# Kernel tuning notes

Hardware: AMD Instinct MI355X
Metric: run time of the kernel (lower is better)

Reference implementation:

```python
import jax, jax.numpy as jnp
import numpy as np

BN_EPS = 1e-5


def _gin_layer(x, src, dst, n_nodes, W1, b1, W2, b2, gamma, beta):
    # GINConv with eps=0: z_i = x_i + sum_{(j->i) in E} x_j, then 2-layer MLP
    agg = jax.ops.segment_sum(x[src], dst, num_segments=n_nodes)  # [N, d]
    z = x + agg
    z = jax.nn.relu(z @ W1 + b1) @ W2 + b2
    # BatchNorm1d (training mode: biased batch statistics over node dim)
    mean = jnp.mean(z, axis=0)
    var = jnp.var(z, axis=0)
    z = (z - mean) * jax.lax.rsqrt(var + BN_EPS) * gamma + beta
    return jax.nn.relu(z)  # dropout p=0 -> identity


def setup_inputs() -> dict:
    key = jax.random.key(0)
    ks = jax.random.split(key, 8)
    N, E, D, L = 50000, 800000, 128, 2
    h = jax.random.normal(ks[0], (N, D), dtype=jnp.float32)
    edge_index = jax.random.randint(ks[1], (2, E), 0, N, dtype=jnp.int64)
    scale = 1.0 / np.sqrt(D)
    W1 = jax.random.normal(ks[2], (L, D, D), dtype=jnp.float32) * scale
    b1 = jax.random.normal(ks[3], (L, D), dtype=jnp.float32) * 0.01
    W2 = jax.random.normal(ks[4], (L, D, D), dtype=jnp.float32) * scale
    b2 = jax.random.normal(ks[5], (L, D), dtype=jnp.float32) * 0.01
    gamma = jnp.ones((L, D), dtype=jnp.float32)
    beta = jnp.zeros((L, D), dtype=jnp.float32)
    return {"h": h, "edge_index": edge_index, "W1": W1, "b1": b1,
            "W2": W2, "b2": b2, "gamma": gamma, "beta": beta}


def reference(h, edge_index, W1, b1, W2, b2, gamma, beta):
    src, dst = edge_index[0], edge_index[1]
    n_nodes = h.shape[0]
    n_layers = W1.shape[0]
    outs = []
    x = h
    for i in range(n_layers):
        x = _gin_layer(x, src, dst, n_nodes, W1[i], b1[i], W2[i], b2[i], gamma[i], beta[i])
        outs.append(x)
    return jnp.stack(outs)  # [L, N, D] == hs[1:]
```

## Files before the change

kernel.cpp:

```cpp
#include <hip/hip_runtime.h>

#define D 128
#define BN_EPS 1e-5f

typedef __attribute__((ext_vector_type(8))) short short8;
typedef __attribute__((ext_vector_type(4))) float f32x4;

__device__ inline unsigned short f2bf(float f) {
    union { float f; unsigned int u; } v; v.f = f;
    unsigned int u = v.u;
    unsigned int r = (u + 0x7FFFu + ((u >> 16) & 1u)) >> 16;
    return (unsigned short)r;
}

__device__ inline float bfbits2f(unsigned int bits) {
    union { unsigned int u; float f; } v; v.u = bits;
    return v.f;
}

__device__ inline float4 bf2f4(uint2 v) {
    float4 r;
    r.x = bfbits2f(v.x << 16);
    r.y = bfbits2f(v.x & 0xFFFF0000u);
    r.z = bfbits2f(v.y << 16);
    r.w = bfbits2f(v.y & 0xFFFF0000u);
    return r;
}

__global__ void hist_rank(const int* __restrict__ dst, int* __restrict__ cnt,
                          int* __restrict__ rank, int E) {
    int e = blockIdx.x * blockDim.x + threadIdx.x;
    if (e >= E) return;
    rank[e] = atomicAdd(&cnt[dst[e]], 1);
}

__global__ void reduce_cnt(const int* __restrict__ cnt, int* __restrict__ bsum, int n) {
    __shared__ int s[256];
    int tid = threadIdx.x;
    int i = blockIdx.x * 256 + tid;
    s[tid] = (i < n) ? cnt[i] : 0;
    __syncthreads();
    for (int ofs = 128; ofs > 0; ofs >>= 1) {
        if (tid < ofs) s[tid] += s[tid + ofs];
        __syncthreads();
    }
    if (tid == 0) bsum[blockIdx.x] = s[0];
}

__global__ void scan_bsums(const int* __restrict__ bsum, int* __restrict__ blockOff,
                           int* __restrict__ offN, int nb) {
    __shared__ int s[256];
    int tid = threadIdx.x;
    int v = (tid < nb) ? bsum[tid] : 0;
    s[tid] = v;
    __syncthreads();
    for (int ofs = 1; ofs < 256; ofs <<= 1) {
        int t = (tid >= ofs) ? s[tid - ofs] : 0;
        __syncthreads();
        s[tid] += t;
        __syncthreads();
    }
    if (tid < nb) blockOff[tid] = s[tid] - v;
    if (tid == nb - 1) *offN = s[tid];
}

__global__ void scan_partial(const int* __restrict__ cnt, int* __restrict__ off,
                             const int* __restrict__ blockOff, int n) {
    __shared__ int s[256];
    int tid = threadIdx.x;
    int i = blockIdx.x * 256 + tid;
    int v = (i < n) ? cnt[i] : 0;
    s[tid] = v;
    __syncthreads();
    for (int ofs = 1; ofs < 256; ofs <<= 1) {
        int t = (tid >= ofs) ? s[tid - ofs] : 0;
        __syncthreads();
        s[tid] += t;
        __syncthreads();
    }
    if (i < n) off[i] = blockOff[blockIdx.x] + s[tid] - v;
}

template<typename IdxT>
__global__ void fill2(const int* __restrict__ src, const int* __restrict__ dst,
                      const int* __restrict__ rank, const int* __restrict__ off,
                      IdxT* __restrict__ eidx, int E) {
    int e = blockIdx.x * blockDim.x + threadIdx.x;
    if (e >= E) return;
    eidx[off[dst[e]] + rank[e]] = (IdxT)src[e];
}

__global__ void wprep(const float* __restrict__ W1, const float* __restrict__ W2,
                      unsigned short* __restrict__ Wt, int L) {
    int idx = blockIdx.x * 256 + threadIdx.x;
    int m = idx >> 14;
    int rem = idx & 16383;
    int c = rem >> 7, k = rem & 127;
    const float* W = (m < L) ? (W1 + (size_t)m * D * D) : (W2 + (size_t)(m - L) * D * D);
    Wt[(size_t)m * D * D + c * D + k] = f2bf(W[k * D + c]);
}

__global__ void x2bf(const float* __restrict__ x, unsigned short* __restrict__ xb, int n8) {
    int i = blockIdx.x * 256 + threadIdx.x;
    if (i >= n8) return;
    float4 a = reinterpret_cast<const float4*>(x)[2 * i];
    float4 b = reinterpret_cast<const float4*>(x)[2 * i + 1];
    uint4 o;
    o.x = (unsigned)f2bf(a.x) | ((unsigned)f2bf(a.y) << 16);
    o.y = (unsigned)f2bf(a.z) | ((unsigned)f2bf(a.w) << 16);
    o.z = (unsigned)f2bf(b.x) | ((unsigned)f2bf(b.y) << 16);
    o.w = (unsigned)f2bf(b.z) | ((unsigned)f2bf(b.w) << 16);
    reinterpret_cast<uint4*>(xb)[i] = o;
}

template<typename IdxT>
__global__ __launch_bounds__(256) void gather_bf(
        const unsigned short* __restrict__ xb, const int* __restrict__ off,
        const IdxT* __restrict__ eidx, unsigned short* __restrict__ zb, int N) {
    int t = blockIdx.x * blockDim.x + threadIdx.x;
    int node = t >> 5;
    if (node >= N) return;
    int lane = t & 31;
    int beg = off[node], end = off[node + 1];
    float4 acc = bf2f4(*reinterpret_cast<const uint2*>(xb + (size_t)node * D + lane * 4));
    int e = beg;
    for (; e + 2 <= end; e += 2) {
        int s0 = (int)eidx[e], s1 = (int)eidx[e + 1];
        uint2 v0 = *reinterpret_cast<const uint2*>(xb + (size_t)s0 * D + lane * 4);
        uint2 v1 = *reinterpret_cast<const uint2*>(xb + (size_t)s1 * D + lane * 4);
        float4 f0 = bf2f4(v0), f1 = bf2f4(v1);
        acc.x += f0.x + f1.x; acc.y += f0.y + f1.y;
        acc.z += f0.z + f1.z; acc.w += f0.w + f1.w;
    }
    if (e < end) {
        int s0 = (int)eidx[e];
        float4 f0 = bf2f4(*reinterpret_cast<const uint2*>(xb + (size_t)s0 * D + lane * 4));
        acc.x += f0.x; acc.y += f0.y; acc.z += f0.z; acc.w += f0.w;
    }
    uint2 o;
    o.x = (unsigned)f2bf(acc.x) | ((unsigned)f2bf(acc.y) << 16);
    o.y = (unsigned)f2bf(acc.z) | ((unsigned)f2bf(acc.w) << 16);
    *reinterpret_cast<uint2*>(zb + (size_t)node * D + lane * 4) = o;
}

__global__ __launch_bounds__(256) void gemm1_mfma(
        const unsigned short* __restrict__ A, const unsigned short* __restrict__ Wt,
        const float* __restrict__ bias, unsigned short* __restrict__ Out, int N) {
    const int tid = threadIdx.x;
    const int lane = tid & 63, wv = tid >> 6;
    const int r0 = blockIdx.x * 128 + wv * 32;
    const int koff = (lane >> 4) << 3;
    const int col = lane & 15;

    int ar0 = r0 + col;       if (ar0 >= N) ar0 = N - 1;
    int ar1 = r0 + 16 + col;  if (ar1 >= N) ar1 = N - 1;
    const unsigned short* ap0 = A + (size_t)ar0 * D + koff;
    const unsigned short* ap1 = A + (size_t)ar1 * D + koff;
    const unsigned short* wp  = Wt + (size_t)col * D + koff;

    f32x4 acc[2][8];
    #pragma unroll
    for (int ct = 0; ct < 8; ct++) {
        float b = bias[ct * 16 + col];
        acc[0][ct] = (f32x4){b, b, b, b};
        acc[1][ct] = (f32x4){b, b, b, b};
    }
    #pragma unroll
    for (int ks = 0; ks < 4; ks++) {
        short8 a0 = *reinterpret_cast<const short8*>(ap0 + ks * 32);
        short8 a1 = *reinterpret_cast<const short8*>(ap1 + ks * 32);
        #pragma unroll
        for (int ct = 0; ct < 8; ct++) {
            short8 bfr = *reinterpret_cast<const short8*>(wp + (size_t)ct * 16 * D + ks * 32);
            acc[0][ct] = __builtin_amdgcn_mfma_f32_16x16x32_bf16(a0, bfr, acc[0][ct], 0, 0, 0);
            acc[1][ct] = __builtin_amdgcn_mfma_f32_16x16x32_bf16(a1, bfr, acc[1][ct], 0, 0, 0);
        }
    }
    #pragma unroll
    for (int t = 0; t < 2; t++) {
        #pragma unroll
        for (int ct = 0; ct < 8; ct++) {
            #pragma unroll
            for (int r = 0; r < 4; r++) {
                int row = r0 + t * 16 + ((lane >> 4) << 2) + r;
                if (row < N)
                    Out[(size_t)row * D + ct * 16 + col] = f2bf(fmaxf(acc[t][ct][r], 0.f));
            }
        }
    }
}

__global__ __launch_bounds__(256) void gemm2_mfma(
        const unsigned short* __restrict__ A, const unsigned short* __restrict__ Wt,
        const float* __restrict__ bias, float* __restrict__ Out,
        float* __restrict__ gstats, int N) {
    __shared__ float sStat[2 * D];
    const int tid = threadIdx.x;
    if (tid < 2 * D) sStat[tid] = 0.f;
    __syncthreads();

    const int lane = tid & 63, wv = tid >> 6;
    const int r0 = blockIdx.x * 128 + wv * 32;
    const int koff = (lane >> 4) << 3;
    const int col = lane & 15;

    int ar0 = r0 + col;       if (ar0 >= N) ar0 = N - 1;
    int ar1 = r0 + 16 + col;  if (ar1 >= N) ar1 = N - 1;
    const unsigned short* ap0 = A + (size_t)ar0 * D + koff;
    const unsigned short* ap1 = A + (size_t)ar1 * D + koff;
    const unsigned short* wp  = Wt + (size_t)col * D + koff;

    f32x4 acc[2][8];
    #pragma unroll
    for (int ct = 0; ct < 8; ct++) {
        float b = bias[ct * 16 + col];
        acc[0][ct] = (f32x4){b, b, b, b};
        acc[1][ct] = (f32x4){b, b, b, b};
    }
    #pragma unroll
    for (int ks = 0; ks < 4; ks++) {
        short8 a0 = *reinterpret_cast<const short8*>(ap0 + ks * 32);
        short8 a1 = *reinterpret_cast<const short8*>(ap1 + ks * 32);
        #pragma unroll
        for (int ct = 0; ct < 8; ct++) {
            short8 bfr = *reinterpret_cast<const short8*>(wp + (size_t)ct * 16 * D + ks * 32);
            acc[0][ct] = __builtin_amdgcn_mfma_f32_16x16x32_bf16(a0, bfr, acc[0][ct], 0, 0, 0);
            acc[1][ct] = __builtin_amdgcn_mfma_f32_16x16x32_bf16(a1, bfr, acc[1][ct], 0, 0, 0);
        }
    }
    #pragma unroll
    for (int ct = 0; ct < 8; ct++) {
        float s = 0.f, q = 0.f;
        #pragma unroll
        for (int t = 0; t < 2; t++) {
            #pragma unroll
            for (int r = 0; r < 4; r++) {
                int row = r0 + t * 16 + ((lane >> 4) << 2) + r;
                float v = acc[t][ct][r];
                if (row < N) {
                    Out[(size_t)row * D + ct * 16 + col] = v;
                    s += v; q += v * v;
                }
            }
        }
        s += __shfl_xor(s, 16); q += __shfl_xor(q, 16);
        s += __shfl_xor(s, 32); q += __shfl_xor(q, 32);
        if (lane < 16) {
            atomicAdd(&sStat[ct * 16 + lane], s);
            atomicAdd(&sStat[D + ct * 16 + lane], q);
        }
    }
    __syncthreads();
    if (tid < 2 * D) atomicAdd(&gstats[tid], sStat[tid]);
}

__global__ void bn_relu_bf(float* __restrict__ y, unsigned short* __restrict__ xb,
                           const float* __restrict__ stats,
                           const float* __restrict__ gamma, const float* __restrict__ beta,
                           int N, int emit_bf) {
    int i = blockIdx.x * blockDim.x + threadIdx.x;
    int n4 = N * D / 4;
    if (i >= n4) return;
    int c0 = (i << 2) & (D - 1);
    float4 v = reinterpret_cast<float4*>(y)[i];
    float o[4] = {v.x, v.y, v.z, v.w};
    float invN = 1.0f / (float)N;
    #pragma unroll
    for (int j = 0; j < 4; j++) {
        int c = c0 + j;
        float mean = stats[c] * invN;
        float var  = stats[D + c] * invN - mean * mean;
        float sc = rsqrtf(var + BN_EPS) * gamma[c];
        float t = (o[j] - mean) * sc + beta[c];
        o[j] = fmaxf(t, 0.f);
    }
    float4 r; r.x = o[0]; r.y = o[1]; r.z = o[2]; r.w = o[3];
    reinterpret_cast<float4*>(y)[i] = r;
    if (emit_bf) {
        uint2 ob;
        ob.x = (unsigned)f2bf(o[0]) | ((unsigned)f2bf(o[1]) << 16);
        ob.y = (unsigned)f2bf(o[2]) | ((unsigned)f2bf(o[3]) << 16);
        reinterpret_cast<uint2*>(xb)[i] = ob;
    }
}

extern "C" void kernel_launch(void* const* d_in, const int* in_sizes, int n_in,
                              void* d_out, int out_size, void* d_ws, size_t ws_size,
                              hipStream_t stream) {
    const float* h     = (const float*)d_in[0];
    const int*   ei    = (const int*)d_in[1];
    const float* W1    = (const float*)d_in[2];
    const float* b1    = (const float*)d_in[3];
    const float* W2    = (const float*)d_in[4];
    const float* b2    = (const float*)d_in[5];
    const float* gamma = (const float*)d_in[6];
    const float* beta  = (const float*)d_in[7];
    float* out = (float*)d_out;

    const int N = in_sizes[0] / D;
    const int E = in_sizes[1] / 2;
    const int L = in_sizes[2] / (D * D);
    const int nb = (N + 255) / 256;

    unsigned short* zb  = (unsigned short*)d_ws;
    unsigned short* xb  = zb + (size_t)N * D;
    unsigned short* Wt  = xb + (size_t)N * D;
    float* stats = (float*)(Wt + (size_t)2 * L * D * D);
    int* cnt      = (int*)(stats + (size_t)L * 2 * D);
    int* off      = cnt + N;
    int* bsum     = off + N + 1;
    int* blockOff = bsum + nb;
    int* rank     = blockOff + nb;
    void* eidx    = (void*)(rank + E);

    const int* src = ei;
    const int* dst = ei + E;

    const int n4 = N * D / 4;
    const int n8 = N * D / 8;
    const int ewBlocks = (E + 255) / 256;
    const int gatherBlocks = (N * 32 + 255) / 256;
    const int gemmBlocks = (N + 127) / 128;
    const int bnBlocks = (n4 + 255) / 256;
    const int wprepBlocks = (2 * L * D * D) / 256;
    const bool small = (N <= 65535);

    hipMemsetAsync(cnt, 0, N * sizeof(int), stream);
    hipMemsetAsync(stats, 0, (size_t)L * 2 * D * sizeof(float), stream);
    wprep<<<wprepBlocks, 256, 0, stream>>>(W1, W2, Wt, L);
    x2bf<<<(n8 + 255) / 256, 256, 0, stream>>>(h, xb, n8);

    hist_rank<<<ewBlocks, 256, 0, stream>>>(dst, cnt, rank, E);
    reduce_cnt<<<nb, 256, 0, stream>>>(cnt, bsum, N);
    scan_bsums<<<1, 256, 0, stream>>>(bsum, blockOff, off + N, nb);
    scan_partial<<<nb, 256, 0, stream>>>(cnt, off, blockOff, N);
    if (small)
        fill2<unsigned short><<<ewBlocks, 256, 0, stream>>>(src, dst, rank, off,
                                                            (unsigned short*)eidx, E);
    else
        fill2<int><<<ewBlocks, 256, 0, stream>>>(src, dst, rank, off, (int*)eidx, E);

    for (int l = 0; l < L; l++) {
        float* y = out + (size_t)l * N * D;

        if (small)
            gather_bf<unsigned short><<<gatherBlocks, 256, 0, stream>>>(
                xb, off, (const unsigned short*)eidx, zb, N);
        else
            gather_bf<int><<<gatherBlocks, 256, 0, stream>>>(
                xb, off, (const int*)eidx, zb, N);
        gemm1_mfma<<<gemmBlocks, 256, 0, stream>>>(zb, Wt + (size_t)l * D * D,
                                                   b1 + (size_t)l * D, zb, N);
        gemm2_mfma<<<gemmBlocks, 256, 0, stream>>>(zb, Wt + (size_t)(L + l) * D * D,
                                                   b2 + (size_t)l * D, y, stats + (size_t)l * 2 * D, N);
        bn_relu_bf<<<bnBlocks, 256, 0, stream>>>(y, xb, stats + (size_t)l * 2 * D,
                                                 gamma + (size_t)l * D, beta + (size_t)l * D,
                                                 N, (l + 1 < L) ? 1 : 0);
    }
}
```

Before: 240.5 us.

## Fuse neighbor gather and both MLP GEMMs into one kernel via LDS tile

Replaces the separate gather, gemm1 and gemm2 kernels with one fused kernel per layer. Each block gathers 128 node rows into a swizzled 32KB LDS tile, runs the first GEMM with ReLU back into LDS, then runs the second GEMM and accumulates BN statistics. This removes the global round trips of the aggregated and hidden bf16 activations and two launches per layer. In exchange, occupancy drops because of the large LDS use and high register pressure, and the irregular gather phase gets less latency hiding, since each wave now walks 16 rows serially.

```diff
diff --git a/kernel.cpp b/kernel.cpp
--- a/kernel.cpp
+++ b/kernel.cpp
@@ -114,66 +114,78 @@
 }
 
 template<typename IdxT>
-__global__ __launch_bounds__(256) void gather_bf(
+__global__ __launch_bounds__(256) void fused_layer(
         const unsigned short* __restrict__ xb, const int* __restrict__ off,
-        const IdxT* __restrict__ eidx, unsigned short* __restrict__ zb, int N) {
-    int t = blockIdx.x * blockDim.x + threadIdx.x;
-    int node = t >> 5;
-    if (node >= N) return;
-    int lane = t & 31;
-    int beg = off[node], end = off[node + 1];
-    float4 acc = bf2f4(*reinterpret_cast<const uint2*>(xb + (size_t)node * D + lane * 4));
-    int e = beg;
-    for (; e + 2 <= end; e += 2) {
-        int s0 = (int)eidx[e], s1 = (int)eidx[e + 1];
-        uint2 v0 = *reinterpret_cast<const uint2*>(xb + (size_t)s0 * D + lane * 4);
-        uint2 v1 = *reinterpret_cast<const uint2*>(xb + (size_t)s1 * D + lane * 4);
-        float4 f0 = bf2f4(v0), f1 = bf2f4(v1);
-        acc.x += f0.x + f1.x; acc.y += f0.y + f1.y;
-        acc.z += f0.z + f1.z; acc.w += f0.w + f1.w;
-    }
-    if (e < end) {
-        int s0 = (int)eidx[e];
-        float4 f0 = bf2f4(*reinterpret_cast<const uint2*>(xb + (size_t)s0 * D + lane * 4));
-        acc.x += f0.x; acc.y += f0.y; acc.z += f0.z; acc.w += f0.w;
-    }
-    uint2 o;
-    o.x = (unsigned)f2bf(acc.x) | ((unsigned)f2bf(acc.y) << 16);
-    o.y = (unsigned)f2bf(acc.z) | ((unsigned)f2bf(acc.w) << 16);
-    *reinterpret_cast<uint2*>(zb + (size_t)node * D + lane * 4) = o;
-}
-
-__global__ __launch_bounds__(256) void gemm1_mfma(
-        const unsigned short* __restrict__ A, const unsigned short* __restrict__ Wt,
-        const float* __restrict__ bias, unsigned short* __restrict__ Out, int N) {
+        const IdxT* __restrict__ eidx,
+        const unsigned short* __restrict__ Wt1, const float* __restrict__ b1,
+        const unsigned short* __restrict__ Wt2, const float* __restrict__ b2,
+        float* __restrict__ Out, float* __restrict__ gstats, int N) {
+    __shared__ __align__(16) char sZ[128 * 256];
+    __shared__ float sStat[2 * D];
     const int tid = threadIdx.x;
     const int lane = tid & 63, wv = tid >> 6;
-    const int r0 = blockIdx.x * 128 + wv * 32;
-    const int koff = (lane >> 4) << 3;
+    const int row0 = blockIdx.x * 128;
+
+    sStat[tid] = 0.f;
+
+    {
+        const int lane32 = lane & 31;
+        const int sub = lane >> 5;
+        for (int it = 0; it < 16; it++) {
+            int lrow = wv * 32 + it * 2 + sub;
+            int node = row0 + lrow;
+            float4 acc = make_float4(0.f, 0.f, 0.f, 0.f);
+            if (node < N) {
+                acc = bf2f4(*reinterpret_cast<const uint2*>(xb + (size_t)node * D + lane32 * 4));
+                int beg = off[node], end = off[node + 1];
+                int e = beg;
+                for (; e + 2 <= end; e += 2) {
+                    int s0 = (int)eidx[e], s1 = (int)eidx[e + 1];
+                    float4 f0 = bf2f4(*reinterpret_cast<const uint2*>(xb + (size_t)s0 * D + lane32 * 4));
+                    float4 f1 = bf2f4(*reinterpret_cast<const uint2*>(xb + (size_t)s1 * D + lane32 * 4));
+                    acc.x += f0.x + f1.x; acc.y += f0.y + f1.y;
+                    acc.z += f0.z + f1.z; acc.w += f0.w + f1.w;
+                }
+                if (e < end) {
+                    int s0 = (int)eidx[e];
+                    float4 f0 = bf2f4(*reinterpret_cast<const uint2*>(xb + (size_t)s0 * D + lane32 * 4));
+                    acc.x += f0.x; acc.y += f0.y; acc.z += f0.z; acc.w += f0.w;
+                }
+            }
+            uint2 o;
+            o.x = (unsigned)f2bf(acc.x) | ((unsigned)f2bf(acc.y) << 16);
+            o.y = (unsigned)f2bf(acc.z) | ((unsigned)f2bf(acc.w) << 16);
+            *reinterpret_cast<uint2*>(sZ + lrow * 256 + ((lane32 * 8) ^ ((lrow & 7) << 4))) = o;
+        }
+    }
+    __syncthreads();
+
     const int col = lane & 15;
-
-    int ar0 = r0 + col;       if (ar0 >= N) ar0 = N - 1;
-    int ar1 = r0 + 16 + col;  if (ar1 >= N) ar1 = N - 1;
-    const unsigned short* ap0 = A + (size_t)ar0 * D + koff;
-    const unsigned short* ap1 = A + (size_t)ar1 * D + koff;
-    const unsigned short* wp  = Wt + (size_t)col * D + koff;
-
-    f32x4 acc[2][8];
+    const int kq = lane >> 4;
+    const int lrow0 = wv * 32 + col;
+    const int lrow1 = wv * 32 + 16 + col;
+
+    f32x4 acc1[2][8];
     #pragma unroll
     for (int ct = 0; ct < 8; ct++) {
-        float b = bias[ct * 16 + col];
-        acc[0][ct] = (f32x4){b, b, b, b};
-        acc[1][ct] = (f32x4){b, b, b, b};
-    }
-    #pragma unroll
-    for (int ks = 0; ks < 4; ks++) {
-        short8 a0 = *reinterpret_cast<const short8*>(ap0 + ks * 32);
-        short8 a1 = *reinterpret_cast<const short8*>(ap1 + ks * 32);
+        float b = b1[ct * 16 + col];
+        acc1[0][ct] = (f32x4){b, b, b, b};
+        acc1[1][ct] = (f32x4){b, b, b, b};
+    }
+    {
+        const unsigned short* wp = Wt1 + (size_t)col * D + kq * 8;
         #pragma unroll
-        for (int ct = 0; ct < 8; ct++) {
-            short8 bfr = *reinterpret_cast<const short8*>(wp + (size_t)ct * 16 * D + ks * 32);
-            acc[0][ct] = __builtin_amdgcn_mfma_f32_16x16x32_bf16(a0, bfr, acc[0][ct], 0, 0, 0);
-            acc[1][ct] = __builtin_amdgcn_mfma_f32_16x16x32_bf16(a1, bfr, acc[1][ct], 0, 0, 0);
+        for (int ks = 0; ks < 4; ks++) {
+            short8 a0 = *reinterpret_cast<const short8*>(
+                sZ + lrow0 * 256 + ((kq * 16 + ks * 64) ^ ((lrow0 & 7) << 4)));
+            short8 a1 = *reinterpret_cast<const short8*>(
+                sZ + lrow1 * 256 + ((kq * 16 + ks * 64) ^ ((lrow1 & 7) << 4)));
+            #pragma unroll
+            for (int ct = 0; ct < 8; ct++) {
+                short8 bfr = *reinterpret_cast<const short8*>(wp + (size_t)ct * 16 * D + ks * 32);
+                acc1[0][ct] = __builtin_amdgcn_mfma_f32_16x16x32_bf16(a0, bfr, acc1[0][ct], 0, 0, 0);
+                acc1[1][ct] = __builtin_amdgcn_mfma_f32_16x16x32_bf16(a1, bfr, acc1[1][ct], 0, 0, 0);
+            }
         }
     }
     #pragma unroll
@@ -182,50 +194,36 @@
         for (int ct = 0; ct < 8; ct++) {
             #pragma unroll
             for (int r = 0; r < 4; r++) {
-                int row = r0 + t * 16 + ((lane >> 4) << 2) + r;
-                if (row < N)
-                    Out[(size_t)row * D + ct * 16 + col] = f2bf(fmaxf(acc[t][ct][r], 0.f));
-            }
-        }
-    }
-}
-
-__global__ __launch_bounds__(256) void gemm2_mfma(
-        const unsigned short* __restrict__ A, const unsigned short* __restrict__ Wt,
-        const float* __restrict__ bias, float* __restrict__ Out,
-        float* __restrict__ gstats, int N) {
-    __shared__ float sStat[2 * D];
-    const int tid = threadIdx.x;
-    if (tid < 2 * D) sStat[tid] = 0.f;
-    __syncthreads();
-
-    const int lane = tid & 63, wv = tid >> 6;
-    const int r0 = blockIdx.x * 128 + wv * 32;
-    const int koff = (lane >> 4) << 3;
-    const int col = lane & 15;
-
-    int ar0 = r0 + col;       if (ar0 >= N) ar0 = N - 1;
-    int ar1 = r0 + 16 + col;  if (ar1 >= N) ar1 = N - 1;
-    const unsigned short* ap0 = A + (size_t)ar0 * D + koff;
-    const unsigned short* ap1 = A + (size_t)ar1 * D + koff;
-    const unsigned short* wp  = Wt + (size_t)col * D + koff;
-
-    f32x4 acc[2][8];
+                int lrow = wv * 32 + t * 16 + kq * 4 + r;
+                int c = ct * 16 + col;
+                unsigned short hv = f2bf(fmaxf(acc1[t][ct][r], 0.f));
+                *reinterpret_cast<unsigned short*>(
+                    sZ + lrow * 256 + ((c * 2) ^ ((lrow & 7) << 4))) = hv;
+            }
+        }
+    }
+
+    f32x4 acc2[2][8];
     #pragma unroll
     for (int ct = 0; ct < 8; ct++) {
-        float b = bias[ct * 16 + col];
-        acc[0][ct] = (f32x4){b, b, b, b};
-        acc[1][ct] = (f32x4){b, b, b, b};
-    }
-    #pragma unroll
-    for (int ks = 0; ks < 4; ks++) {
-        short8 a0 = *reinterpret_cast<const short8*>(ap0 + ks * 32);
-        short8 a1 = *reinterpret_cast<const short8*>(ap1 + ks * 32);
+        float b = b2[ct * 16 + col];
+        acc2[0][ct] = (f32x4){b, b, b, b};
+        acc2[1][ct] = (f32x4){b, b, b, b};
+    }
+    {
+        const unsigned short* wp = Wt2 + (size_t)col * D + kq * 8;
         #pragma unroll
-        for (int ct = 0; ct < 8; ct++) {
-            short8 bfr = *reinterpret_cast<const short8*>(wp + (size_t)ct * 16 * D + ks * 32);
-            acc[0][ct] = __builtin_amdgcn_mfma_f32_16x16x32_bf16(a0, bfr, acc[0][ct], 0, 0, 0);
-            acc[1][ct] = __builtin_amdgcn_mfma_f32_16x16x32_bf16(a1, bfr, acc[1][ct], 0, 0, 0);
+        for (int ks = 0; ks < 4; ks++) {
+            short8 a0 = *reinterpret_cast<const short8*>(
+                sZ + lrow0 * 256 + ((kq * 16 + ks * 64) ^ ((lrow0 & 7) << 4)));
+            short8 a1 = *reinterpret_cast<const short8*>(
+                sZ + lrow1 * 256 + ((kq * 16 + ks * 64) ^ ((lrow1 & 7) << 4)));
+            #pragma unroll
+            for (int ct = 0; ct < 8; ct++) {
+                short8 bfr = *reinterpret_cast<const short8*>(wp + (size_t)ct * 16 * D + ks * 32);
+                acc2[0][ct] = __builtin_amdgcn_mfma_f32_16x16x32_bf16(a0, bfr, acc2[0][ct], 0, 0, 0);
+                acc2[1][ct] = __builtin_amdgcn_mfma_f32_16x16x32_bf16(a1, bfr, acc2[1][ct], 0, 0, 0);
+            }
         }
     }
     #pragma unroll
@@ -235,8 +233,8 @@
         for (int t = 0; t < 2; t++) {
             #pragma unroll
             for (int r = 0; r < 4; r++) {
-                int row = r0 + t * 16 + ((lane >> 4) << 2) + r;
-                float v = acc[t][ct][r];
+                int row = row0 + wv * 32 + t * 16 + kq * 4 + r;
+                float v = acc2[t][ct][r];
                 if (row < N) {
                     Out[(size_t)row * D + ct * 16 + col] = v;
                     s += v; q += v * v;
@@ -251,7 +249,7 @@
         }
     }
     __syncthreads();
-    if (tid < 2 * D) atomicAdd(&gstats[tid], sStat[tid]);
+    atomicAdd(&gstats[tid], sStat[tid]);
 }
 
 __global__ void bn_relu_bf(float* __restrict__ y, unsigned short* __restrict__ xb,
@@ -302,8 +300,7 @@
     const int L = in_sizes[2] / (D * D);
     const int nb = (N + 255) / 256;
 
-    unsigned short* zb  = (unsigned short*)d_ws;
-    unsigned short* xb  = zb + (size_t)N * D;
+    unsigned short* xb  = (unsigned short*)d_ws;
     unsigned short* Wt  = xb + (size_t)N * D;
     float* stats = (float*)(Wt + (size_t)2 * L * D * D);
     int* cnt      = (int*)(stats + (size_t)L * 2 * D);
@@ -319,8 +316,7 @@
     const int n4 = N * D / 4;
     const int n8 = N * D / 8;
     const int ewBlocks = (E + 255) / 256;
-    const int gatherBlocks = (N * 32 + 255) / 256;
-    const int gemmBlocks = (N + 127) / 128;
+    const int fusedBlocks = (N + 127) / 128;
     const int bnBlocks = (n4 + 255) / 256;
     const int wprepBlocks = (2 * L * D * D) / 256;
     const bool small = (N <= 65535);
@@ -342,17 +338,18 @@
 
     for (int l = 0; l < L; l++) {
         float* y = out + (size_t)l * N * D;
+        const unsigned short* Wt1 = Wt + (size_t)l * D * D;
+        const unsigned short* Wt2 = Wt + (size_t)(L + l) * D * D;
 
         if (small)
-            gather_bf<unsigned short><<<gatherBlocks, 256, 0, stream>>>(
-                xb, off, (const unsigned short*)eidx, zb, N);
+            fused_layer<unsigned short><<<fusedBlocks, 256, 0, stream>>>(
+                xb, off, (const unsigned short*)eidx, Wt1, b1 + (size_t)l * D,
+                Wt2, b2 + (size_t)l * D, y, stats + (size_t)l * 2 * D, N);
         else
-            gather_bf<int><<<gatherBlocks, 256, 0, stream>>>(
-                xb, off, (const int*)eidx, zb, N);
-        gemm1_mfma<<<gemmBlocks, 256, 0, stream>>>(zb, Wt + (size_t)l * D * D,
-                                                   b1 + (size_t)l * D, zb, N);
-        gemm2_mfma<<<gemmBlocks, 256, 0, stream>>>(zb, Wt + (size_t)(L + l) * D * D,
-                                                   b2 + (size_t)l * D, y, stats + (size_t)l * 2 * D, N);
+            fused_layer<int><<<fusedBlocks, 256, 0, stream>>>(
+                xb, off, (const int*)eidx, Wt1, b1 + (size_t)l * D,
+                Wt2, b2 + (size_t)l * D, y, stats + (size_t)l * 2 * D, N);
+
         bn_relu_bf<<<bnBlocks, 256, 0, stream>>>(y, xb, stats + (size_t)l * 2 * D,
                                                  gamma + (size_t)l * D, beta + (size_t)l * D,
                                                  N, (l + 1 < L) ? 1 : 0);
```

Result: slower. 346.9 us (+44.2%).

## Fuse the two MLP GEMMs into one kernel with swizzled LDS intermediate

Applied to the files above, without the earlier changes.

Replaces the separate gemm1 and gemm2 kernels with a single mlp_mfma kernel. The ReLU hidden activation is kept in swizzled shared memory per wave instead of round-tripping through global memory as bf16. Each wave now handles 16 rows instead of 32, and blocks cover 64 rows. This removes one launch and the global write and read of the N×128 intermediate, at the cost of half the weight-fragment reuse per wave and more blocks.

```diff
diff --git a/kernel.cpp b/kernel.cpp
--- a/kernel.cpp
+++ b/kernel.cpp
@@ -143,104 +143,81 @@
     *reinterpret_cast<uint2*>(zb + (size_t)node * D + lane * 4) = o;
 }
 
-__global__ __launch_bounds__(256) void gemm1_mfma(
-        const unsigned short* __restrict__ A, const unsigned short* __restrict__ Wt,
-        const float* __restrict__ bias, unsigned short* __restrict__ Out, int N) {
+__global__ __launch_bounds__(256) void mlp_mfma(
+        const unsigned short* __restrict__ A,
+        const unsigned short* __restrict__ Wt1, const float* __restrict__ bias1,
+        const unsigned short* __restrict__ Wt2, const float* __restrict__ bias2,
+        float* __restrict__ Out, float* __restrict__ gstats, int N) {
+    __shared__ __align__(16) char sZ1[4 * 4096];
+    __shared__ float sStat[2 * D];
     const int tid = threadIdx.x;
     const int lane = tid & 63, wv = tid >> 6;
-    const int r0 = blockIdx.x * 128 + wv * 32;
-    const int koff = (lane >> 4) << 3;
+    const int row0 = blockIdx.x * 64 + wv * 16;
     const int col = lane & 15;
-
-    int ar0 = r0 + col;       if (ar0 >= N) ar0 = N - 1;
-    int ar1 = r0 + 16 + col;  if (ar1 >= N) ar1 = N - 1;
-    const unsigned short* ap0 = A + (size_t)ar0 * D + koff;
-    const unsigned short* ap1 = A + (size_t)ar1 * D + koff;
-    const unsigned short* wp  = Wt + (size_t)col * D + koff;
-
-    f32x4 acc[2][8];
+    const int kq = lane >> 4;
+
+    sStat[tid] = 0.f;
+    __syncthreads();
+
+    int arow = row0 + col; if (arow >= N) arow = N - 1;
+    const unsigned short* ap  = A + (size_t)arow * D + kq * 8;
+    const unsigned short* wp1 = Wt1 + (size_t)col * D + kq * 8;
+    const unsigned short* wp2 = Wt2 + (size_t)col * D + kq * 8;
+    char* zbase = sZ1 + wv * 4096;
+
+    f32x4 acc1[8];
     #pragma unroll
     for (int ct = 0; ct < 8; ct++) {
-        float b = bias[ct * 16 + col];
-        acc[0][ct] = (f32x4){b, b, b, b};
-        acc[1][ct] = (f32x4){b, b, b, b};
+        float b = bias1[ct * 16 + col];
+        acc1[ct] = (f32x4){b, b, b, b};
     }
     #pragma unroll
     for (int ks = 0; ks < 4; ks++) {
-        short8 a0 = *reinterpret_cast<const short8*>(ap0 + ks * 32);
-        short8 a1 = *reinterpret_cast<const short8*>(ap1 + ks * 32);
+        short8 a = *reinterpret_cast<const short8*>(ap + ks * 32);
         #pragma unroll
         for (int ct = 0; ct < 8; ct++) {
-            short8 bfr = *reinterpret_cast<const short8*>(wp + (size_t)ct * 16 * D + ks * 32);
-            acc[0][ct] = __builtin_amdgcn_mfma_f32_16x16x32_bf16(a0, bfr, acc[0][ct], 0, 0, 0);
-            acc[1][ct] = __builtin_amdgcn_mfma_f32_16x16x32_bf16(a1, bfr, acc[1][ct], 0, 0, 0);
-        }
-    }
-    #pragma unroll
-    for (int t = 0; t < 2; t++) {
+            short8 bfr = *reinterpret_cast<const short8*>(wp1 + (size_t)ct * 16 * D + ks * 32);
+            acc1[ct] = __builtin_amdgcn_mfma_f32_16x16x32_bf16(a, bfr, acc1[ct], 0, 0, 0);
+        }
+    }
+    #pragma unroll
+    for (int ct = 0; ct < 8; ct++) {
+        #pragma unroll
+        for (int r = 0; r < 4; r++) {
+            int lrow = kq * 4 + r;
+            int c = ct * 16 + col;
+            *reinterpret_cast<unsigned short*>(
+                zbase + lrow * 256 + ((c * 2) ^ ((lrow & 7) << 4))) =
+                f2bf(fmaxf(acc1[ct][r], 0.f));
+        }
+    }
+
+    f32x4 acc2[8];
+    #pragma unroll
+    for (int ct = 0; ct < 8; ct++) {
+        float b = bias2[ct * 16 + col];
+        acc2[ct] = (f32x4){b, b, b, b};
+    }
+    #pragma unroll
+    for (int ks = 0; ks < 4; ks++) {
+        short8 a = *reinterpret_cast<const short8*>(
+            zbase + col * 256 + ((kq * 16 + ks * 64) ^ ((col & 7) << 4)));
         #pragma unroll
         for (int ct = 0; ct < 8; ct++) {
-            #pragma unroll
-            for (int r = 0; r < 4; r++) {
-                int row = r0 + t * 16 + ((lane >> 4) << 2) + r;
-                if (row < N)
-                    Out[(size_t)row * D + ct * 16 + col] = f2bf(fmaxf(acc[t][ct][r], 0.f));
-            }
-        }
-    }
-}
-
-__global__ __launch_bounds__(256) void gemm2_mfma(
-        const unsigned short* __restrict__ A, const unsigned short* __restrict__ Wt,
-        const float* __restrict__ bias, float* __restrict__ Out,
-        float* __restrict__ gstats, int N) {
-    __shared__ float sStat[2 * D];
-    const int tid = threadIdx.x;
-    if (tid < 2 * D) sStat[tid] = 0.f;
-    __syncthreads();
-
-    const int lane = tid & 63, wv = tid >> 6;
-    const int r0 = blockIdx.x * 128 + wv * 32;
-    const int koff = (lane >> 4) << 3;
-    const int col = lane & 15;
-
-    int ar0 = r0 + col;       if (ar0 >= N) ar0 = N - 1;
-    int ar1 = r0 + 16 + col;  if (ar1 >= N) ar1 = N - 1;
-    const unsigned short* ap0 = A + (size_t)ar0 * D + koff;
-    const unsigned short* ap1 = A + (size_t)ar1 * D + koff;
-    const unsigned short* wp  = Wt + (size_t)col * D + koff;
-
-    f32x4 acc[2][8];
-    #pragma unroll
-    for (int ct = 0; ct < 8; ct++) {
-        float b = bias[ct * 16 + col];
-        acc[0][ct] = (f32x4){b, b, b, b};
-        acc[1][ct] = (f32x4){b, b, b, b};
-    }
-    #pragma unroll
-    for (int ks = 0; ks < 4; ks++) {
-        short8 a0 = *reinterpret_cast<const short8*>(ap0 + ks * 32);
-        short8 a1 = *reinterpret_cast<const short8*>(ap1 + ks * 32);
-        #pragma unroll
-        for (int ct = 0; ct < 8; ct++) {
-            short8 bfr = *reinterpret_cast<const short8*>(wp + (size_t)ct * 16 * D + ks * 32);
-            acc[0][ct] = __builtin_amdgcn_mfma_f32_16x16x32_bf16(a0, bfr, acc[0][ct], 0, 0, 0);
-            acc[1][ct] = __builtin_amdgcn_mfma_f32_16x16x32_bf16(a1, bfr, acc[1][ct], 0, 0, 0);
+            short8 bfr = *reinterpret_cast<const short8*>(wp2 + (size_t)ct * 16 * D + ks * 32);
+            acc2[ct] = __builtin_amdgcn_mfma_f32_16x16x32_bf16(a, bfr, acc2[ct], 0, 0, 0);
         }
     }
     #pragma unroll
     for (int ct = 0; ct < 8; ct++) {
         float s = 0.f, q = 0.f;
         #pragma unroll
-        for (int t = 0; t < 2; t++) {
-            #pragma unroll
-            for (int r = 0; r < 4; r++) {
-                int row = r0 + t * 16 + ((lane >> 4) << 2) + r;
-                float v = acc[t][ct][r];
-                if (row < N) {
-                    Out[(size_t)row * D + ct * 16 + col] = v;
-                    s += v; q += v * v;
-                }
+        for (int r = 0; r < 4; r++) {
+            int row = row0 + kq * 4 + r;
+            float v = acc2[ct][r];
+            if (row < N) {
+                Out[(size_t)row * D + ct * 16 + col] = v;
+                s += v; q += v * v;
             }
         }
         s += __shfl_xor(s, 16); q += __shfl_xor(q, 16);
@@ -251,7 +228,7 @@
         }
     }
     __syncthreads();
-    if (tid < 2 * D) atomicAdd(&gstats[tid], sStat[tid]);
+    atomicAdd(&gstats[tid], sStat[tid]);
 }
 
 __global__ void bn_relu_bf(float* __restrict__ y, unsigned short* __restrict__ xb,
@@ -320,7 +297,7 @@
     const int n8 = N * D / 8;
     const int ewBlocks = (E + 255) / 256;
     const int gatherBlocks = (N * 32 + 255) / 256;
-    const int gemmBlocks = (N + 127) / 128;
+    const int mlpBlocks = (N + 63) / 64;
     const int bnBlocks = (n4 + 255) / 256;
     const int wprepBlocks = (2 * L * D * D) / 256;
     const bool small = (N <= 65535);
@@ -342,6 +319,8 @@
 
     for (int l = 0; l < L; l++) {
         float* y = out + (size_t)l * N * D;
+        const unsigned short* Wt1 = Wt + (size_t)l * D * D;
+        const unsigned short* Wt2 = Wt + (size_t)(L + l) * D * D;
 
         if (small)
             gather_bf<unsigned short><<<gatherBlocks, 256, 0, stream>>>(
@@ -349,10 +328,11 @@
         else
             gather_bf<int><<<gatherBlocks, 256, 0, stream>>>(
                 xb, off, (const int*)eidx, zb, N);
-        gemm1_mfma<<<gemmBlocks, 256, 0, stream>>>(zb, Wt + (size_t)l * D * D,
-                                                   b1 + (size_t)l * D, zb, N);
-        gemm2_mfma<<<gemmBlocks, 256, 0, stream>>>(zb, Wt + (size_t)(L + l) * D * D,
-                                                   b2 + (size_t)l * D, y, stats + (size_t)l * 2 * D, N);
+
+        mlp_mfma<<<mlpBlocks, 256, 0, stream>>>(zb, Wt1, b1 + (size_t)l * D,
+                                                Wt2, b2 + (size_t)l * D,
+                                                y, stats + (size_t)l * 2 * D, N);
+
         bn_relu_bf<<<bnBlocks, 256, 0, stream>>>(y, xb, stats + (size_t)l * 2 * D,
                                                  gamma + (size_t)l * D, beta + (size_t)l * D,
                                                  N, (l + 1 < L) ? 1 : 0);
```

After: 270.7 us. 12.5% more time.

## Merge setup kernels and fuse block-sum scan via last-block pattern; nontemporal stores

Applied to the files above, without the earlier changes.

Two memsets and the weight-transpose and input-cast kernels become one grid-stride prep kernel. The reduce and block-offset scan kernels merge into one, where the last block to finish, found through an atomic counter and threadfences, does the scan. Nontemporal stores are used for the CSR fill and for the gather output. Together this cuts four launches plus two memsets, and in exchange adds atomic and fence overhead, a fixed 1024-block prep grid, and possible cache effects from the nontemporal stores.

```diff
diff --git a/kernel.cpp b/kernel.cpp
--- a/kernel.cpp
+++ b/kernel.cpp
@@ -27,6 +27,36 @@
     return r;
 }
 
+__global__ void prep_all(const float* __restrict__ W1, const float* __restrict__ W2,
+                         unsigned short* __restrict__ Wt,
+                         const float* __restrict__ h, unsigned short* __restrict__ xb,
+                         int* __restrict__ cnt, float* __restrict__ stats,
+                         int* __restrict__ done, int N, int L, int n8) {
+    const int nth = gridDim.x * blockDim.x;
+    const int tid = blockIdx.x * blockDim.x + threadIdx.x;
+    if (tid == 0) *done = 0;
+    for (int i = tid; i < N; i += nth) cnt[i] = 0;
+    for (int i = tid; i < 2 * D * L; i += nth) stats[i] = 0.f;
+    const int nw = 2 * L * D * D;
+    for (int idx = tid; idx < nw; idx += nth) {
+        int m = idx >> 14;
+        int rem = idx & 16383;
+        int c = rem >> 7, k = rem & 127;
+        const float* W = (m < L) ? (W1 + (size_t)m * D * D) : (W2 + (size_t)(m - L) * D * D);
+        Wt[(size_t)m * D * D + c * D + k] = f2bf(W[k * D + c]);
+    }
+    for (int i = tid; i < n8; i += nth) {
+        float4 a = reinterpret_cast<const float4*>(h)[2 * i];
+        float4 b = reinterpret_cast<const float4*>(h)[2 * i + 1];
+        uint4 o;
+        o.x = (unsigned)f2bf(a.x) | ((unsigned)f2bf(a.y) << 16);
+        o.y = (unsigned)f2bf(a.z) | ((unsigned)f2bf(a.w) << 16);
+        o.z = (unsigned)f2bf(b.x) | ((unsigned)f2bf(b.y) << 16);
+        o.w = (unsigned)f2bf(b.z) | ((unsigned)f2bf(b.w) << 16);
+        reinterpret_cast<uint4*>(xb)[i] = o;
+    }
+}
+
 __global__ void hist_rank(const int* __restrict__ dst, int* __restrict__ cnt,
                           int* __restrict__ rank, int E) {
     int e = blockIdx.x * blockDim.x + threadIdx.x;
@@ -34,8 +64,11 @@
     rank[e] = atomicAdd(&cnt[dst[e]], 1);
 }
 
-__global__ void reduce_cnt(const int* __restrict__ cnt, int* __restrict__ bsum, int n) {
+__global__ void reduce_scan(const int* __restrict__ cnt, int* __restrict__ bsum,
+                            int* __restrict__ blockOff, int* __restrict__ offN,
+                            int* __restrict__ done, int n, int nb) {
     __shared__ int s[256];
+    __shared__ int isLast;
     int tid = threadIdx.x;
     int i = blockIdx.x * 256 + tid;
     s[tid] = (i < n) ? cnt[i] : 0;
@@ -44,24 +77,26 @@
         if (tid < ofs) s[tid] += s[tid + ofs];
         __syncthreads();
     }
-    if (tid == 0) bsum[blockIdx.x] = s[0];
-}
-
-__global__ void scan_bsums(const int* __restrict__ bsum, int* __restrict__ blockOff,
-                           int* __restrict__ offN, int nb) {
-    __shared__ int s[256];
-    int tid = threadIdx.x;
-    int v = (tid < nb) ? bsum[tid] : 0;
-    s[tid] = v;
-    __syncthreads();
-    for (int ofs = 1; ofs < 256; ofs <<= 1) {
-        int t = (tid >= ofs) ? s[tid - ofs] : 0;
+    if (tid == 0) {
+        bsum[blockIdx.x] = s[0];
+        __threadfence();
+        isLast = (atomicAdd(done, 1) == nb - 1) ? 1 : 0;
+    }
+    __syncthreads();
+    if (isLast) {
+        __threadfence();
+        int v = (tid < nb) ? bsum[tid] : 0;
+        s[tid] = v;
         __syncthreads();
-        s[tid] += t;
-        __syncthreads();
-    }
-    if (tid < nb) blockOff[tid] = s[tid] - v;
-    if (tid == nb - 1) *offN = s[tid];
+        for (int ofs = 1; ofs < 256; ofs <<= 1) {
+            int t2 = (tid >= ofs) ? s[tid - ofs] : 0;
+            __syncthreads();
+            s[tid] += t2;
+            __syncthreads();
+        }
+        if (tid < nb) blockOff[tid] = s[tid] - v;
+        if (tid == nb - 1) *offN = s[tid];
+    }
 }
 
 __global__ void scan_partial(const int* __restrict__ cnt, int* __restrict__ off,
@@ -87,30 +122,7 @@
                       IdxT* __restrict__ eidx, int E) {
     int e = blockIdx.x * blockDim.x + threadIdx.x;
     if (e >= E) return;
-    eidx[off[dst[e]] + rank[e]] = (IdxT)src[e];
-}
-
-__global__ void wprep(const float* __restrict__ W1, const float* __restrict__ W2,
-                      unsigned short* __restrict__ Wt, int L) {
-    int idx = blockIdx.x * 256 + threadIdx.x;
-    int m = idx >> 14;
-    int rem = idx & 16383;
-    int c = rem >> 7, k = rem & 127;
-    const float* W = (m < L) ? (W1 + (size_t)m * D * D) : (W2 + (size_t)(m - L) * D * D);
-    Wt[(size_t)m * D * D + c * D + k] = f2bf(W[k * D + c]);
-}
-
-__global__ void x2bf(const float* __restrict__ x, unsigned short* __restrict__ xb, int n8) {
-    int i = blockIdx.x * 256 + threadIdx.x;
-    if (i >= n8) return;
-    float4 a = reinterpret_cast<const float4*>(x)[2 * i];
-    float4 b = reinterpret_cast<const float4*>(x)[2 * i + 1];
-    uint4 o;
-    o.x = (unsigned)f2bf(a.x) | ((unsigned)f2bf(a.y) << 16);
-    o.y = (unsigned)f2bf(a.z) | ((unsigned)f2bf(a.w) << 16);
-    o.z = (unsigned)f2bf(b.x) | ((unsigned)f2bf(b.y) << 16);
-    o.w = (unsigned)f2bf(b.z) | ((unsigned)f2bf(b.w) << 16);
-    reinterpret_cast<uint4*>(xb)[i] = o;
+    __builtin_nontemporal_store((IdxT)src[e], &eidx[off[dst[e]] + rank[e]]);
 }
 
 template<typename IdxT>
@@ -137,10 +149,11 @@
         float4 f0 = bf2f4(*reinterpret_cast<const uint2*>(xb + (size_t)s0 * D + lane * 4));
         acc.x += f0.x; acc.y += f0.y; acc.z += f0.z; acc.w += f0.w;
     }
-    uint2 o;
-    o.x = (unsigned)f2bf(acc.x) | ((unsigned)f2bf(acc.y) << 16);
-    o.y = (unsigned)f2bf(acc.z) | ((unsigned)f2bf(acc.w) << 16);
-    *reinterpret_cast<uint2*>(zb + (size_t)node * D + lane * 4) = o;
+    unsigned long long packed =
+        ((unsigned long long)((unsigned)f2bf(acc.z) | ((unsigned)f2bf(acc.w) << 16)) << 32) |
+        (unsigned long long)((unsigned)f2bf(acc.x) | ((unsigned)f2bf(acc.y) << 16));
+    __builtin_nontemporal_store(packed,
+        reinterpret_cast<unsigned long long*>(zb + (size_t)node * D + lane * 4));
 }
 
 __global__ __launch_bounds__(256) void gemm1_mfma(
@@ -310,7 +323,8 @@
     int* off      = cnt + N;
     int* bsum     = off + N + 1;
     int* blockOff = bsum + nb;
-    int* rank     = blockOff + nb;
+    int* done     = blockOff + nb;
+    int* rank     = done + 1;
     void* eidx    = (void*)(rank + E);
 
     const int* src = ei;
@@ -322,17 +336,12 @@
     const int gatherBlocks = (N * 32 + 255) / 256;
     const int gemmBlocks = (N + 127) / 128;
     const int bnBlocks = (n4 + 255) / 256;
-    const int wprepBlocks = (2 * L * D * D) / 256;
     const bool small = (N <= 65535);
 
-    hipMemsetAsync(cnt, 0, N * sizeof(int), stream);
-    hipMemsetAsync(stats, 0, (size_t)L * 2 * D * sizeof(float), stream);
-    wprep<<<wprepBlocks, 256, 0, stream>>>(W1, W2, Wt, L);
-    x2bf<<<(n8 + 255) / 256, 256, 0, stream>>>(h, xb, n8);
+    prep_all<<<1024, 256, 0, stream>>>(W1, W2, Wt, h, xb, cnt, stats, done, N, L, n8);
 
     hist_rank<<<ewBlocks, 256, 0, stream>>>(dst, cnt, rank, E);
-    reduce_cnt<<<nb, 256, 0, stream>>>(cnt, bsum, N);
-    scan_bsums<<<1, 256, 0, stream>>>(bsum, blockOff, off + N, nb);
+    reduce_scan<<<nb, 256, 0, stream>>>(cnt, bsum, blockOff, off + N, done, N, nb);
     scan_partial<<<nb, 256, 0, stream>>>(cnt, off, blockOff, N);
     if (small)
         fill2<unsigned short><<<ewBlocks, 256, 0, stream>>>(src, dst, rank, off,
@@ -342,6 +351,8 @@
 
     for (int l = 0; l < L; l++) {
         float* y = out + (size_t)l * N * D;
+        const unsigned short* Wt1 = Wt + (size_t)l * D * D;
+        const unsigned short* Wt2 = Wt + (size_t)(L + l) * D * D;
 
         if (small)
             gather_bf<unsigned short><<<gatherBlocks, 256, 0, stream>>>(
@@ -349,10 +360,10 @@
         else
             gather_bf<int><<<gatherBlocks, 256, 0, stream>>>(
                 xb, off, (const int*)eidx, zb, N);
-        gemm1_mfma<<<gemmBlocks, 256, 0, stream>>>(zb, Wt + (size_t)l * D * D,
-                                                   b1 + (size_t)l * D, zb, N);
-        gemm2_mfma<<<gemmBlocks, 256, 0, stream>>>(zb, Wt + (size_t)(L + l) * D * D,
-                                                   b2 + (size_t)l * D, y, stats + (size_t)l * 2 * D, N);
+
+        gemm1_mfma<<<gemmBlocks, 256, 0, stream>>>(zb, Wt1, b1 + (size_t)l * D, zb, N);
+        gemm2_mfma<<<gemmBlocks, 256, 0, stream>>>(zb, Wt2, b2 + (size_t)l * D,
+                                                   y, stats + (size_t)l * 2 * D, N);
         bn_relu_bf<<<bnBlocks, 256, 0, stream>>>(y, xb, stats + (size_t)l * 2 * D,
                                                  gamma + (size_t)l * D, beta + (size_t)l * D,
                                                  N, (l + 1 < L) ? 1 : 0);
```

After: 249.2 us. 3.6% more time.
